# Optimization experiments

Measured on AMD Instinct MI355X. Metric: run time of the kernel, lower is better.

The kernel has to match this reference:

```python
import jax, jax.numpy as jnp
import numpy as np

TOPK = 10
MIN_SIM = 0.8
MIN_VOTES = 0.0
REMOVE_INNER_THR = 0.8
NUM_CLASSES = 1000
D, C, N = 256, 256, 500000


def setup_inputs() -> dict:
    key = jax.random.key(0)
    k1, k2, k3, k4, k5 = jax.random.split(key, 5)
    # query descriptors, L2-normalized (cosine similarity, matches min_sim=0.8 semantics)
    q = jax.random.normal(k1, (D, C), dtype=jnp.float32)
    q = q / jnp.linalg.norm(q, axis=1, keepdims=True)
    # database descriptors + integer place_id stored as the last float column
    x = jax.random.normal(k2, (N, C), dtype=jnp.float32)
    x = x / jnp.linalg.norm(x, axis=1, keepdims=True)
    ids = jax.random.randint(k3, (N,), 0, NUM_CLASSES).astype(jnp.float32)
    places_db = jnp.concatenate([x, ids[:, None]], axis=1)  # (N, C+1)
    # valid xyxy boxes in a ~1000px image
    xy = jax.random.uniform(k4, (D, 2), dtype=jnp.float32) * 800.0
    wh = jax.random.uniform(k5, (D, 2), dtype=jnp.float32) * 200.0 + 1.0
    final_boxes = jnp.concatenate([xy, xy + wh], axis=1)  # (D, 4)
    return {"final_boxes": final_boxes, "descriptors": q, "places_db": places_db}


def _remove_overlapping_boxes(boxes, labels, thr):
    # boxes: (D,4) xyxy, labels: (D,) int32
    b = boxes.astype(jnp.float32)
    areas = (b[:, 2] - b[:, 0]) * (b[:, 3] - b[:, 1])  # (D,)
    xi1 = jnp.maximum(b[:, None, 0], b[None, :, 0])
    yi1 = jnp.maximum(b[:, None, 1], b[None, :, 1])
    xi2 = jnp.minimum(b[:, None, 2], b[None, :, 2])
    yi2 = jnp.minimum(b[:, None, 3], b[None, :, 3])
    inter = jnp.clip(xi2 - xi1, 0.0) * jnp.clip(yi2 - yi1, 0.0)  # (D,D)
    area_i = areas[:, None]
    area_j = areas[None, :]
    area_small = jnp.minimum(area_i, area_j)
    overlap = jnp.where(area_small > 0, inter / jnp.where(area_small > 0, area_small, 1.0), 0.0)
    same_lbl = (labels[:, None] == labels[None, :]) & (labels[:, None] >= 0)
    n = boxes.shape[0]
    non_diag = ~jnp.eye(n, dtype=bool)
    mask_pair = same_lbl & (overlap >= thr) & non_diag
    bigger_i = area_i > area_j
    remove_i = jnp.any(mask_pair & bigger_i, axis=1)
    remove_j = jnp.any(mask_pair & ~bigger_i, axis=0)
    remove = remove_i | remove_j
    return jnp.where(remove, jnp.full_like(labels, -1), labels)


def reference(final_boxes, descriptors, places_db):
    X = places_db[:, :-1]                       # (N, C)
    idx = places_db[:, -1].astype(jnp.int32)    # (N,)
    sims = descriptors @ X.T                    # (D, N)
    top_sims, top_idx = jax.lax.top_k(sims, TOPK)  # (D, K)
    top_ids = idx[top_idx]                      # (D, K)
    mask_sim = top_sims >= MIN_SIM              # (D, K)
    one_hot = jax.nn.one_hot(top_ids, NUM_CLASSES, dtype=jnp.float32)  # (D, K, Ncls)
    vote_counts = jnp.sum(one_hot * mask_sim[..., None].astype(jnp.float32), axis=1)  # (D, Ncls)
    majority_counts = jnp.max(vote_counts, axis=1)
    majority_ids = jnp.argmax(vote_counts, axis=1).astype(jnp.int32)
    valid_votes = jnp.sum(mask_sim, axis=1).astype(jnp.float32)
    vote_ratio = jnp.where(valid_votes > 0, majority_counts / jnp.where(valid_votes > 0, valid_votes, 1.0), 0.0)
    valid = (majority_counts > 0) & (vote_ratio >= MIN_VOTES)
    results = jnp.where(valid, majority_ids, jnp.full_like(majority_ids, -1))
    results = _remove_overlapping_boxes(final_boxes, results, REMOVE_INNER_THR)
    match = (top_ids == results[:, None]) & mask_sim
    sim_scores = jnp.max(jnp.where(match, top_sims, jnp.zeros_like(top_sims)), axis=1)  # (D,)
    return (final_boxes, sim_scores, results)
```

## Files before the change

### kernel.cpp

```cpp
#include <hip/hip_runtime.h>
#include <stdint.h>

#define NQ      256
#define NC      256
#define NDB     500000
#define ROWLEN  257
#define MIN_SIM_F 0.8f
#define NMS_THR   0.8f
#define CAP     64
#define TILE    16
#define NTILES  (NDB / TILE)
#define BLK     512
#define GEMM_GRID 512

typedef __bf16 bf16x8 __attribute__((ext_vector_type(8)));
typedef float  f32x4  __attribute__((ext_vector_type(4)));

union BU { unsigned short u[8]; bf16x8 v; };

__device__ __forceinline__ unsigned short f2bf(float f) {
    uint32_t u = __float_as_uint(f);
    u += 0x7FFFu + ((u >> 16) & 1u);
    return (unsigned short)(u >> 16);
}

__global__ void init_counts(int* cnt) { cnt[threadIdx.x] = 0; }

__global__ __launch_bounds__(BLK, 4) void gemm_filter(
    const float* __restrict__ q, const float* __restrict__ db,
    int* __restrict__ cnt, float* __restrict__ csim, int* __restrict__ cidx)
{
    __shared__ __align__(16) unsigned short Bs[2][TILE][264];

    const int tid  = threadIdx.x;
    const int wave = tid >> 6;
    const int lane = tid & 63;
    const int quad = lane >> 4;
    const int l16  = lane & 15;

    bf16x8 a[2][8];
    #pragma unroll
    for (int f = 0; f < 2; ++f) {
        const int m = wave * 32 + f * 16 + l16;
        const float* qrow = q + m * NC;
        #pragma unroll
        for (int s = 0; s < 8; ++s) {
            const int k0 = s * 32 + quad * 8;
            BU u;
            #pragma unroll
            for (int j = 0; j < 8; ++j) u.u[j] = f2bf(qrow[k0 + j]);
            a[f][s] = u.v;
        }
    }

    f32x4 r0, r1, rx;

    auto LOAD = [&](int tile) {
        const f32x4* src = (const f32x4*)(db + (size_t)tile * (TILE * ROWLEN));
        r0 = src[tid];
        r1 = src[tid + 512];
        if (tid < 4) rx = src[1024 + tid];
    };

    auto STORE1 = [&](unsigned short* dst, f32x4 v, int idx) {
        const int f   = idx * 4;
        const int row = f / 257;
        const int col = f - row * 257;
        const int base = row * 264 + col;
        #pragma unroll
        for (int j = 0; j < 4; ++j) {
            const int adr = base + j + ((col + j >= 257) ? 7 : 0);
            dst[adr] = f2bf(v[j]);
        }
    };

    auto WRITE = [&](int nb) {
        unsigned short* dst = &Bs[nb][0][0];
        STORE1(dst, r0, tid);
        STORE1(dst, r1, tid + 512);
        if (tid < 4) STORE1(dst, rx, 1024 + tid);
    };

    auto COMPUTE = [&](int cb, int tile) {
        const f32x4 zero = {0.f, 0.f, 0.f, 0.f};
        f32x4 acc[2] = {zero, zero};
        #pragma unroll
        for (int s = 0; s < 8; ++s) {
            const bf16x8 b = *(const bf16x8*)&Bs[cb][l16][s * 32 + quad * 8];
            acc[0] = __builtin_amdgcn_mfma_f32_16x16x32_bf16(a[0][s], b, acc[0], 0, 0, 0);
            acc[1] = __builtin_amdgcn_mfma_f32_16x16x32_bf16(a[1][s], b, acc[1], 0, 0, 0);
        }
        float mx = acc[0][0];
        #pragma unroll
        for (int fm = 0; fm < 2; ++fm)
            #pragma unroll
            for (int rr = 0; rr < 4; ++rr) mx = fmaxf(mx, acc[fm][rr]);
        if (mx >= MIN_SIM_F) {
            #pragma unroll
            for (int fm = 0; fm < 2; ++fm) {
                #pragma unroll
                for (int rr = 0; rr < 4; ++rr) {
                    const float sv = acc[fm][rr];
                    if (sv >= MIN_SIM_F) {
                        const int qi   = wave * 32 + fm * 16 + quad * 4 + rr;
                        const int rowg = tile * TILE + l16;
                        const int pos = atomicAdd(&cnt[qi], 1);
                        if (pos < CAP) {
                            csim[qi * CAP + pos] = sv;
                            cidx[qi * CAP + pos] = rowg;
                        }
                    }
                }
            }
        }
    };

    int tile = blockIdx.x;
    LOAD(tile);
    WRITE(0);
    __syncthreads();
    int buf = 0;
    for (;;) {
        const int next = tile + GEMM_GRID;
        const bool more = (next < NTILES);
        if (more) LOAD(next);
        COMPUTE(buf, tile);
        if (!more) break;
        WRITE(buf ^ 1);
        __syncthreads();
        buf ^= 1;
        tile = next;
    }
}

__device__ __forceinline__ bool better(float s1, int i1, float s2, int i2) {
    return (s1 > s2) || (s1 == s2 && i1 < i2);
}

__global__ __launch_bounds__(256) void postprocess(
    const float* __restrict__ boxes, const float* __restrict__ db,
    const int* __restrict__ cnt, const float* __restrict__ csim,
    const int* __restrict__ cidx, float* __restrict__ out)
{
    __shared__ int   lab[NQ];
    __shared__ float area_s[NQ];
    __shared__ float bx[NQ][4];

    const int q = threadIdx.x;

    float s10[10]; int i10[10];
    int k = 0;
    int c = cnt[q]; if (c > CAP) c = CAP;
    for (int j = 0; j < c; ++j) {
        const float s = csim[q * CAP + j];
        const int   ix = cidx[q * CAP + j];
        int p;
        if (k < 10) { p = k; ++k; }
        else { if (!better(s, ix, s10[9], i10[9])) continue; p = 9; }
        while (p > 0 && better(s, ix, s10[p - 1], i10[p - 1])) {
            s10[p] = s10[p - 1]; i10[p] = i10[p - 1]; --p;
        }
        s10[p] = s; i10[p] = ix;
    }

    int vid[10];
    for (int j = 0; j < k; ++j) vid[j] = (int)db[(size_t)i10[j] * ROWLEN + (ROWLEN - 1)];
    int best_cnt = 0, best_id = 0x7fffffff;
    for (int j = 0; j < k; ++j) {
        int cj = 0;
        for (int l = 0; l < k; ++l) cj += (vid[l] == vid[j]) ? 1 : 0;
        if (cj > best_cnt || (cj == best_cnt && vid[j] < best_id)) { best_cnt = cj; best_id = vid[j]; }
    }
    const int lq = (best_cnt > 0) ? best_id : -1;
    lab[q] = lq;

    const float x1 = boxes[q * 4 + 0], y1 = boxes[q * 4 + 1];
    const float x2 = boxes[q * 4 + 2], y2 = boxes[q * 4 + 3];
    bx[q][0] = x1; bx[q][1] = y1; bx[q][2] = x2; bx[q][3] = y2;
    const float aq = (x2 - x1) * (y2 - y1);
    area_s[q] = aq;
    __syncthreads();

    bool rem = false;
    if (lq >= 0) {
        for (int p = 0; p < NQ; ++p) {
            if (p == q || lab[p] != lq) continue;
            const float ap = area_s[p];
            if (ap > aq) continue;
            const float xi1 = fmaxf(x1, bx[p][0]);
            const float yi1 = fmaxf(y1, bx[p][1]);
            const float xi2 = fminf(x2, bx[p][2]);
            const float yi2 = fminf(y2, bx[p][3]);
            const float inter = fmaxf(xi2 - xi1, 0.f) * fmaxf(yi2 - yi1, 0.f);
            const float small = fminf(aq, ap);
            const float ov = (small > 0.f) ? inter / small : 0.f;
            if (ov >= NMS_THR) { rem = true; break; }
        }
    }
    const int lq2 = rem ? -1 : lq;

    float score = 0.f;
    if (lq2 >= 0)
        for (int j = 0; j < k; ++j)
            if (vid[j] == lq2) score = fmaxf(score, s10[j]);

    for (int t = q; t < NQ * 4; t += NQ) out[t] = boxes[t];
    out[NQ * 4 + q] = score;
    out[NQ * 5 + q] = (float)lq2;
}

extern "C" void kernel_launch(void* const* d_in, const int* in_sizes, int n_in,
                              void* d_out, int out_size, void* d_ws, size_t ws_size,
                              hipStream_t stream) {
    const float* boxes = (const float*)d_in[0];
    const float* desc  = (const float*)d_in[1];
    const float* db    = (const float*)d_in[2];
    float* out = (float*)d_out;

    int*   cnt  = (int*)d_ws;
    float* csim = (float*)((char*)d_ws + 1024);
    int*   cidx = (int*)((char*)d_ws + 1024 + NQ * CAP * 4);

    init_counts<<<1, 256, 0, stream>>>(cnt);
    gemm_filter<<<GEMM_GRID, BLK, 0, stream>>>(desc, db, cnt, csim, cidx);
    postprocess<<<1, 256, 0, stream>>>(boxes, db, cnt, csim, cidx, out);
}
```

Measured before the change: 684.1 us.

## Use row-aligned vector loads and 32-row tiles in the similarity GEMM filter

Each thread now loads 16 contiguous floats of one database row and writes them to shared memory as two 16-byte packed bf16 stores. This replaces the old flat-index scatter, which needed a per-element division and scalar short stores. The tile grows from 16 to 32 database rows, so each wave runs four MFMA accumulator chains per tile and reuses its A fragments across both halves, halving the syncs per row. In exchange the global loads are only 4-byte aligned because rows are 257 floats long, and register pressure rises from the extra accumulators.

```diff
diff --git a/kernel.cpp b/kernel.cpp
--- a/kernel.cpp
+++ b/kernel.cpp
@@ -8,7 +8,7 @@
 #define MIN_SIM_F 0.8f
 #define NMS_THR   0.8f
 #define CAP     64
-#define TILE    16
+#define TILE    32
 #define NTILES  (NDB / TILE)
 #define BLK     512
 #define GEMM_GRID 512
@@ -37,6 +37,8 @@
     const int lane = tid & 63;
     const int quad = lane >> 4;
     const int l16  = lane & 15;
+    const int rrow = tid >> 4;
+    const int jcol = tid & 15;
 
     bf16x8 a[2][8];
     #pragma unroll
@@ -53,61 +55,65 @@
         }
     }
 
-    f32x4 r0, r1, rx;
+    f32x4 p0, p1, p2, p3;
 
     auto LOAD = [&](int tile) {
-        const f32x4* src = (const f32x4*)(db + (size_t)tile * (TILE * ROWLEN));
-        r0 = src[tid];
-        r1 = src[tid + 512];
-        if (tid < 4) rx = src[1024 + tid];
+        const float* s = db + ((size_t)tile * TILE + rrow) * ROWLEN + jcol * 16;
+        p0 = *(const f32x4*)(s + 0);
+        p1 = *(const f32x4*)(s + 4);
+        p2 = *(const f32x4*)(s + 8);
+        p3 = *(const f32x4*)(s + 12);
     };
 
-    auto STORE1 = [&](unsigned short* dst, f32x4 v, int idx) {
-        const int f   = idx * 4;
-        const int row = f / 257;
-        const int col = f - row * 257;
-        const int base = row * 264 + col;
-        #pragma unroll
-        for (int j = 0; j < 4; ++j) {
-            const int adr = base + j + ((col + j >= 257) ? 7 : 0);
-            dst[adr] = f2bf(v[j]);
-        }
-    };
-
     auto WRITE = [&](int nb) {
-        unsigned short* dst = &Bs[nb][0][0];
-        STORE1(dst, r0, tid);
-        STORE1(dst, r1, tid + 512);
-        if (tid < 4) STORE1(dst, rx, 1024 + tid);
+        union { unsigned short u[8]; uint4 v; } w0, w1;
+        #pragma unroll
+        for (int e = 0; e < 4; ++e) {
+            w0.u[e]     = f2bf(p0[e]);
+            w0.u[4 + e] = f2bf(p1[e]);
+            w1.u[e]     = f2bf(p2[e]);
+            w1.u[4 + e] = f2bf(p3[e]);
+        }
+        uint4* dst = (uint4*)&Bs[nb][rrow][jcol * 16];
+        dst[0] = w0.v;
+        dst[1] = w1.v;
     };
 
     auto COMPUTE = [&](int cb, int tile) {
         const f32x4 zero = {0.f, 0.f, 0.f, 0.f};
-        f32x4 acc[2] = {zero, zero};
+        f32x4 acc[2][2] = {{zero, zero}, {zero, zero}};
         #pragma unroll
         for (int s = 0; s < 8; ++s) {
-            const bf16x8 b = *(const bf16x8*)&Bs[cb][l16][s * 32 + quad * 8];
-            acc[0] = __builtin_amdgcn_mfma_f32_16x16x32_bf16(a[0][s], b, acc[0], 0, 0, 0);
-            acc[1] = __builtin_amdgcn_mfma_f32_16x16x32_bf16(a[1][s], b, acc[1], 0, 0, 0);
-        }
-        float mx = acc[0][0];
+            const bf16x8 b0 = *(const bf16x8*)&Bs[cb][l16][s * 32 + quad * 8];
+            const bf16x8 b1 = *(const bf16x8*)&Bs[cb][16 + l16][s * 32 + quad * 8];
+            acc[0][0] = __builtin_amdgcn_mfma_f32_16x16x32_bf16(a[0][s], b0, acc[0][0], 0, 0, 0);
+            acc[1][0] = __builtin_amdgcn_mfma_f32_16x16x32_bf16(a[1][s], b0, acc[1][0], 0, 0, 0);
+            acc[0][1] = __builtin_amdgcn_mfma_f32_16x16x32_bf16(a[0][s], b1, acc[0][1], 0, 0, 0);
+            acc[1][1] = __builtin_amdgcn_mfma_f32_16x16x32_bf16(a[1][s], b1, acc[1][1], 0, 0, 0);
+        }
+        float mx = acc[0][0][0];
         #pragma unroll
         for (int fm = 0; fm < 2; ++fm)
             #pragma unroll
-            for (int rr = 0; rr < 4; ++rr) mx = fmaxf(mx, acc[fm][rr]);
+            for (int h = 0; h < 2; ++h)
+                #pragma unroll
+                for (int rr = 0; rr < 4; ++rr) mx = fmaxf(mx, acc[fm][h][rr]);
         if (mx >= MIN_SIM_F) {
             #pragma unroll
             for (int fm = 0; fm < 2; ++fm) {
                 #pragma unroll
-                for (int rr = 0; rr < 4; ++rr) {
-                    const float sv = acc[fm][rr];
-                    if (sv >= MIN_SIM_F) {
-                        const int qi   = wave * 32 + fm * 16 + quad * 4 + rr;
-                        const int rowg = tile * TILE + l16;
-                        const int pos = atomicAdd(&cnt[qi], 1);
-                        if (pos < CAP) {
-                            csim[qi * CAP + pos] = sv;
-                            cidx[qi * CAP + pos] = rowg;
+                for (int h = 0; h < 2; ++h) {
+                    #pragma unroll
+                    for (int rr = 0; rr < 4; ++rr) {
+                        const float sv = acc[fm][h][rr];
+                        if (sv >= MIN_SIM_F) {
+                            const int qi   = wave * 32 + fm * 16 + quad * 4 + rr;
+                            const int rowg = tile * TILE + h * 16 + l16;
+                            const int pos = atomicAdd(&cnt[qi], 1);
+                            if (pos < CAP) {
+                                csim[qi * CAP + pos] = sv;
+                                cidx[qi * CAP + pos] = rowg;
+                            }
                         }
                     }
                 }
```

New measurement: 656.5 us. 1.04x faster.
